# Kernel optimization log

Measured on AMD Instinct MI355X. Metric: run time of the kernel, lower is better.

The kernel has to match this reference:

```python
import jax, jax.numpy as jnp
import numpy as np

K = 1.0        # Lorentz manifold curvature parameter
EPS = 1e-7     # arccosh argument clamp (geoopt float32 eps)


def projx(x):
    # Project onto the hyperboloid: x0 = sqrt(K + ||x_1:||^2)
    rest = x[..., 1:]
    x0 = jnp.sqrt(K + jnp.sum(rest * rest, axis=-1, keepdims=True))
    return jnp.concatenate([x0, rest], axis=-1)


def setup_inputs() -> dict:
    key = jax.random.key(0)
    k1, k2 = jax.random.split(key)
    B, C, D = 16384, 2048, 512
    x = jax.random.normal(k1, (B, D), dtype=jnp.float32)
    # ManifoldParameter: random_normal with std = 1/sqrt(n_dim)
    points = jax.random.normal(k2, (C, D), dtype=jnp.float32) * (1.0 / np.sqrt(D))
    return {"x": x, "points": points}


def reference(x, points):
    xp = projx(x)        # (B, D) on hyperboloid
    pp = projx(points)   # (C, D) on hyperboloid
    # Minkowski inner <x,p>_L = -x0*p0 + sum_{i>0} x_i p_i = x.p - 2*x0*p0
    # Computed as a GEMM plus a rank-1 correction (avoids (B,C,D) intermediate).
    inner = xp @ pp.T - 2.0 * jnp.outer(xp[:, 0], pp[:, 0])  # (B, C)
    d = jnp.sqrt(K) * jnp.arccosh(jnp.maximum(-inner / K, 1.0 + EPS))
    return -d  # (B, C) negative Riemannian distances (class logits)
```

## Files before the change

### kernel.cpp

```cpp
#include <hip/hip_runtime.h>
#include <hip/hip_bf16.h>
#include <stdint.h>

#define B_ROWS 16384
#define C_ROWS 2048
#define D_FULL 512
#define KP     512

#define BM 128
#define BN 128
#define BK 64

typedef __attribute__((ext_vector_type(8))) short bf16x8;
typedef __attribute__((ext_vector_type(4))) float f32x4;

typedef __attribute__((address_space(1))) void glb_void;
typedef __attribute__((address_space(3))) void lds_void;

__device__ __forceinline__ void gld16(const void* g, void* l) {
    __builtin_amdgcn_global_load_lds((glb_void*)(uintptr_t)g,
                                     (lds_void*)(uintptr_t)l, 16, 0, 0);
}

__global__ __launch_bounds__(256) void prep_kernel(
    const float* __restrict__ x, const float* __restrict__ pts,
    unsigned short* __restrict__ Abf, unsigned short* __restrict__ Bbf,
    float* __restrict__ xn, float* __restrict__ pn)
{
    int row = blockIdx.x;
    const float* src;
    unsigned short* dst;
    float* nrm;
    if (row < B_ROWS) {
        src = x + (size_t)row * D_FULL;
        dst = Abf + (size_t)row * KP;
        nrm = xn + row;
    } else {
        int r = row - B_ROWS;
        src = pts + (size_t)r * D_FULL;
        dst = Bbf + (size_t)r * KP;
        nrm = pn + r;
    }
    int t = threadIdx.x;
    float v0 = src[2 * t + 1];
    float v1 = (t < 255) ? src[2 * t + 2] : 0.0f;
    __hip_bfloat16 b0 = __float2bfloat16(v0);
    __hip_bfloat16 b1 = __float2bfloat16(v1);
    union { unsigned short u[2]; unsigned int w; } pack;
    pack.u[0] = *(unsigned short*)&b0;
    pack.u[1] = *(unsigned short*)&b1;
    *(unsigned int*)&dst[2 * t] = pack.w;
    float ss = v0 * v0 + v1 * v1;
    #pragma unroll
    for (int off = 32; off > 0; off >>= 1) ss += __shfl_down(ss, off);
    __shared__ float red[4];
    if ((t & 63) == 0) red[t >> 6] = ss;
    __syncthreads();
    if (t == 0) nrm[0] = sqrtf(1.0f + red[0] + red[1] + red[2] + red[3]);
}

__global__ __launch_bounds__(256, 2) void gemm_kernel(
    const unsigned short* __restrict__ A,
    const unsigned short* __restrict__ Bm,
    const float* __restrict__ xn, const float* __restrict__ pn,
    float* __restrict__ out)
{
    __shared__ unsigned short As[2][BM * BK];
    __shared__ unsigned short Bs[2][BN * BK];

    const int tid  = threadIdx.x;
    const int wave = tid >> 6;
    const int lane = tid & 63;
    const int wm   = wave >> 1;
    const int wn   = wave & 1;
    const int lrow = lane & 15;
    const int quad = lane >> 4;

    const int bm0 = blockIdx.x * BM;
    const int bn0 = blockIdx.y * BN;

    const int srow = wave * 32 + (lane >> 3);
    const int scol = (((lane & 7) ^ ((lane >> 3) & 7)) << 3);

    const unsigned short* gA = A  + (size_t)(bm0 + srow) * KP + scol;
    const unsigned short* gB = Bm + (size_t)(bn0 + srow) * KP + scol;

    f32x4 acc[4][4] = {};

    #pragma unroll
    for (int i = 0; i < 4; ++i) {
        gld16(gA + (size_t)(i * 8) * KP, &As[0][(wave * 32 + i * 8) * BK]);
        gld16(gB + (size_t)(i * 8) * KP, &Bs[0][(wave * 32 + i * 8) * BK]);
    }

    #pragma unroll 2
    for (int it = 0; it < KP / BK; ++it) {
        const int buf = it & 1;
        __syncthreads();
        if (it + 1 < KP / BK) {
            const int k1 = (it + 1) * BK;
            #pragma unroll
            for (int i = 0; i < 4; ++i) {
                gld16(gA + (size_t)(i * 8) * KP + k1, &As[buf ^ 1][(wave * 32 + i * 8) * BK]);
                gld16(gB + (size_t)(i * 8) * KP + k1, &Bs[buf ^ 1][(wave * 32 + i * 8) * BK]);
            }
        }
        #pragma unroll
        for (int kk = 0; kk < BK; kk += 32) {
            const int ch0 = kk >> 3;
            bf16x8 af[4], bfr[4];
            #pragma unroll
            for (int mi = 0; mi < 4; ++mi) {
                int r = wm * 64 + mi * 16 + lrow;
                af[mi] = *(const bf16x8*)&As[buf][r * BK + (((ch0 + quad) ^ (lrow & 7)) << 3)];
            }
            #pragma unroll
            for (int ni = 0; ni < 4; ++ni) {
                int r = wn * 64 + ni * 16 + lrow;
                bfr[ni] = *(const bf16x8*)&Bs[buf][r * BK + (((ch0 + quad) ^ (lrow & 7)) << 3)];
            }
            #pragma unroll
            for (int mi = 0; mi < 4; ++mi)
                #pragma unroll
                for (int ni = 0; ni < 4; ++ni)
                    acc[mi][ni] = __builtin_amdgcn_mfma_f32_16x16x32_bf16(
                        af[mi], bfr[ni], acc[mi][ni], 0, 0, 0);
        }
    }

    float pv[4];
    #pragma unroll
    for (int ni = 0; ni < 4; ++ni)
        pv[ni] = pn[bn0 + wn * 64 + ni * 16 + lrow];

    #pragma unroll
    for (int mi = 0; mi < 4; ++mi) {
        #pragma unroll
        for (int r = 0; r < 4; ++r) {
            int row = bm0 + wm * 64 + mi * 16 + quad * 4 + r;
            float xv = xn[row];
            size_t base = (size_t)row * C_ROWS + bn0 + wn * 64 + lrow;
            #pragma unroll
            for (int ni = 0; ni < 4; ++ni) {
                float z = fmaf(xv, pv[ni], -acc[mi][ni][r]);
                z = fmaxf(z, 1.0f + 1e-7f);
                out[base + ni * 16] = -__logf(z + __fsqrt_rn(z * z - 1.0f));
            }
        }
    }
}

extern "C" void kernel_launch(void* const* d_in, const int* in_sizes, int n_in,
                              void* d_out, int out_size, void* d_ws, size_t ws_size,
                              hipStream_t stream) {
    const float* x   = (const float*)d_in[0];
    const float* pts = (const float*)d_in[1];
    float* out = (float*)d_out;

    char* ws = (char*)d_ws;
    unsigned short* Abf = (unsigned short*)ws;
    unsigned short* Bbf = (unsigned short*)(ws + (size_t)B_ROWS * KP * 2);
    float* xn = (float*)(ws + (size_t)(B_ROWS + C_ROWS) * KP * 2);
    float* pn = (float*)((char*)xn + (size_t)B_ROWS * 4);
    (void)in_sizes; (void)n_in; (void)out_size; (void)ws_size;

    prep_kernel<<<B_ROWS + C_ROWS, 256, 0, stream>>>(x, pts, Abf, Bbf, xn, pn);

    dim3 grid(B_ROWS / BM, C_ROWS / BN);
    gemm_kernel<<<grid, 256, 0, stream>>>(Abf, Bbf, xn, pn, out);
}
```

Measured before the change: 192.1 us.

## Use 256x256 tiles with 4-stage LDS pipeline and vectorized prep

Raises the GEMM block tile to 256x256 with 8 waves. A 4-stage global-to-LDS ring at BK=32 replaces the double buffer, with explicit vmcnt waits, barriers, sched barriers and setprio around the MFMA bursts, and the A/B prefetches are split across the two compute halves. The aim is more reuse per loaded byte and better overlap of loads with MFMA work. The prep kernel now handles one row per wave with float4 loads and 16-byte bf16 stores, dropping the block-level shared reduction. In exchange, LDS use grows to 128KB per block, which likely limits occupancy to one block per CU, and the hand-tuned wait counts are fragile.

```diff
diff --git a/kernel.cpp b/kernel.cpp
--- a/kernel.cpp
+++ b/kernel.cpp
@@ -7,9 +7,9 @@
 #define D_FULL 512
 #define KP     512
 
-#define BM 128
-#define BN 128
-#define BK 64
+#define BM 256
+#define BN 256
+#define BK 32
 
 typedef __attribute__((ext_vector_type(8))) short bf16x8;
 typedef __attribute__((ext_vector_type(4))) float f32x4;
@@ -21,13 +21,23 @@
     __builtin_amdgcn_global_load_lds((glb_void*)(uintptr_t)g,
                                      (lds_void*)(uintptr_t)l, 16, 0, 0);
 }
+
+#define WAITV8 asm volatile("s_waitcnt vmcnt(8)" ::: "memory")
+#define WAITV4 asm volatile("s_waitcnt vmcnt(4)" ::: "memory")
+#define WAITV0 asm volatile("s_waitcnt vmcnt(0)" ::: "memory")
+#define WAITL  asm volatile("s_waitcnt lgkmcnt(0)" ::: "memory")
+#define SBAR   __builtin_amdgcn_s_barrier()
+#define SCHEDB __builtin_amdgcn_sched_barrier(0)
 
 __global__ __launch_bounds__(256) void prep_kernel(
     const float* __restrict__ x, const float* __restrict__ pts,
     unsigned short* __restrict__ Abf, unsigned short* __restrict__ Bbf,
     float* __restrict__ xn, float* __restrict__ pn)
 {
-    int row = blockIdx.x;
+    const int wave = threadIdx.x >> 6;
+    const int l    = threadIdx.x & 63;
+    const int row  = blockIdx.x * 4 + wave;
+
     const float* src;
     unsigned short* dst;
     float* nrm;
@@ -36,96 +46,128 @@
         dst = Abf + (size_t)row * KP;
         nrm = xn + row;
     } else {
-        int r = row - B_ROWS;
+        const int r = row - B_ROWS;
         src = pts + (size_t)r * D_FULL;
         dst = Bbf + (size_t)r * KP;
         nrm = pn + r;
     }
-    int t = threadIdx.x;
-    float v0 = src[2 * t + 1];
-    float v1 = (t < 255) ? src[2 * t + 2] : 0.0f;
-    __hip_bfloat16 b0 = __float2bfloat16(v0);
-    __hip_bfloat16 b1 = __float2bfloat16(v1);
-    union { unsigned short u[2]; unsigned int w; } pack;
-    pack.u[0] = *(unsigned short*)&b0;
-    pack.u[1] = *(unsigned short*)&b1;
-    *(unsigned int*)&dst[2 * t] = pack.w;
-    float ss = v0 * v0 + v1 * v1;
+
+    const float4 a = *(const float4*)&src[8 * l];
+    const float4 b = *(const float4*)&src[8 * l + 4];
+    float nx = __shfl_down(a.x, 1);
+    if (l == 63) nx = 0.0f;
+
+    float v[8] = {a.y, a.z, a.w, b.x, b.y, b.z, b.w, nx};
+    float ss = 0.0f;
+    union { unsigned short us[8]; uint4 q; } pk;
+    #pragma unroll
+    for (int j = 0; j < 8; ++j) {
+        ss += v[j] * v[j];
+        __hip_bfloat16 h = __float2bfloat16(v[j]);
+        pk.us[j] = *(unsigned short*)&h;
+    }
+    *(uint4*)&dst[8 * l] = pk.q;
+
     #pragma unroll
     for (int off = 32; off > 0; off >>= 1) ss += __shfl_down(ss, off);
-    __shared__ float red[4];
-    if ((t & 63) == 0) red[t >> 6] = ss;
-    __syncthreads();
-    if (t == 0) nrm[0] = sqrtf(1.0f + red[0] + red[1] + red[2] + red[3]);
-}
-
-__global__ __launch_bounds__(256, 2) void gemm_kernel(
+    if (l == 0) nrm[0] = sqrtf(1.0f + ss);
+}
+
+__global__ __launch_bounds__(512, 2) void gemm_kernel(
     const unsigned short* __restrict__ A,
     const unsigned short* __restrict__ Bm,
     const float* __restrict__ xn, const float* __restrict__ pn,
     float* __restrict__ out)
 {
-    __shared__ unsigned short As[2][BM * BK];
-    __shared__ unsigned short Bs[2][BN * BK];
+    __shared__ unsigned short As[4][8192];
+    __shared__ unsigned short Bs[4][8192];
 
     const int tid  = threadIdx.x;
     const int wave = tid >> 6;
     const int lane = tid & 63;
-    const int wm   = wave >> 1;
-    const int wn   = wave & 1;
+    const int wm   = wave >> 2;
+    const int wn   = wave & 3;
     const int lrow = lane & 15;
     const int quad = lane >> 4;
 
     const int bm0 = blockIdx.x * BM;
     const int bn0 = blockIdx.y * BN;
 
-    const int srow = wave * 32 + (lane >> 3);
-    const int scol = (((lane & 7) ^ ((lane >> 3) & 7)) << 3);
-
-    const unsigned short* gA = A  + (size_t)(bm0 + srow) * KP + scol;
-    const unsigned short* gB = Bm + (size_t)(bn0 + srow) * KP + scol;
-
-    f32x4 acc[4][4] = {};
-
-    #pragma unroll
-    for (int i = 0; i < 4; ++i) {
-        gld16(gA + (size_t)(i * 8) * KP, &As[0][(wave * 32 + i * 8) * BK]);
-        gld16(gB + (size_t)(i * 8) * KP, &Bs[0][(wave * 32 + i * 8) * BK]);
-    }
-
-    #pragma unroll 2
-    for (int it = 0; it < KP / BK; ++it) {
-        const int buf = it & 1;
-        __syncthreads();
-        if (it + 1 < KP / BK) {
-            const int k1 = (it + 1) * BK;
+    const int P  = tid >> 3;
+    const int u  = tid & 7;
+    const int v  = u ^ (P & 7);
+    const int sc = (v >> 1) << 3;
+    const int rb = 2 * P + (v & 1);
+
+    const unsigned short* gA0 = A  + (size_t)(bm0 + rb) * KP + sc;
+    const unsigned short* gA1 = gA0 + (size_t)128 * KP;
+    const unsigned short* gB0 = Bm + (size_t)(bn0 + rb) * KP + sc;
+    const unsigned short* gB1 = gB0 + (size_t)128 * KP;
+
+    #pragma unroll
+    for (int t = 0; t < 3; ++t) {
+        gld16(gA0 + t * BK, &As[t][wave * 512]);
+        gld16(gA1 + t * BK, &As[t][4096 + wave * 512]);
+        gld16(gB0 + t * BK, &Bs[t][wave * 512]);
+        gld16(gB1 + t * BK, &Bs[t][4096 + wave * 512]);
+    }
+
+    const int ccs  = (((quad << 1) | (lrow & 1)) ^ (lrow >> 1)) << 3;
+    const int aoff = (wm * 64 + (lrow >> 1)) * 64 + ccs;
+    const int boff = (wn * 32 + (lrow >> 1)) * 64 + ccs;
+
+    f32x4 acc[8][4] = {};
+
+    #pragma unroll
+    for (int t = 0; t < KP / BK; ++t) {
+        const int s  = t & 3;
+        const int ps = (t + 3) & 3;
+
+        if (t <= 13)      WAITV8;
+        else if (t == 14) WAITV4;
+        else              WAITV0;
+        SBAR; SCHEDB;
+
+        bf16x8 af[4], bfr[4];
+        #pragma unroll
+        for (int mi = 0; mi < 4; ++mi)
+            af[mi] = *(const bf16x8*)&As[s][aoff + mi * 512];
+        #pragma unroll
+        for (int ni = 0; ni < 4; ++ni)
+            bfr[ni] = *(const bf16x8*)&Bs[s][boff + ni * 512];
+        if (t + 3 < KP / BK) {
+            gld16(gA0 + (t + 3) * BK, &As[ps][wave * 512]);
+            gld16(gA1 + (t + 3) * BK, &As[ps][4096 + wave * 512]);
+        }
+        SBAR;
+        WAITL; SCHEDB;
+        __builtin_amdgcn_s_setprio(1);
+        #pragma unroll
+        for (int mi = 0; mi < 4; ++mi)
             #pragma unroll
-            for (int i = 0; i < 4; ++i) {
-                gld16(gA + (size_t)(i * 8) * KP + k1, &As[buf ^ 1][(wave * 32 + i * 8) * BK]);
-                gld16(gB + (size_t)(i * 8) * KP + k1, &Bs[buf ^ 1][(wave * 32 + i * 8) * BK]);
-            }
+            for (int ni = 0; ni < 4; ++ni)
+                acc[mi][ni] = __builtin_amdgcn_mfma_f32_16x16x32_bf16(
+                    af[mi], bfr[ni], acc[mi][ni], 0, 0, 0);
+        __builtin_amdgcn_s_setprio(0);
+        SBAR;
+
+        #pragma unroll
+        for (int mi = 0; mi < 4; ++mi)
+            af[mi] = *(const bf16x8*)&As[s][aoff + (mi + 4) * 512];
+        if (t + 3 < KP / BK) {
+            gld16(gB0 + (t + 3) * BK, &Bs[ps][wave * 512]);
+            gld16(gB1 + (t + 3) * BK, &Bs[ps][4096 + wave * 512]);
         }
-        #pragma unroll
-        for (int kk = 0; kk < BK; kk += 32) {
-            const int ch0 = kk >> 3;
-            bf16x8 af[4], bfr[4];
+        SBAR;
+        WAITL; SCHEDB;
+        __builtin_amdgcn_s_setprio(1);
+        #pragma unroll
+        for (int mi = 0; mi < 4; ++mi)
             #pragma unroll
-            for (int mi = 0; mi < 4; ++mi) {
-                int r = wm * 64 + mi * 16 + lrow;
-                af[mi] = *(const bf16x8*)&As[buf][r * BK + (((ch0 + quad) ^ (lrow & 7)) << 3)];
-            }
-            #pragma unroll
-            for (int ni = 0; ni < 4; ++ni) {
-                int r = wn * 64 + ni * 16 + lrow;
-                bfr[ni] = *(const bf16x8*)&Bs[buf][r * BK + (((ch0 + quad) ^ (lrow & 7)) << 3)];
-            }
-            #pragma unroll
-            for (int mi = 0; mi < 4; ++mi)
-                #pragma unroll
-                for (int ni = 0; ni < 4; ++ni)
-                    acc[mi][ni] = __builtin_amdgcn_mfma_f32_16x16x32_bf16(
-                        af[mi], bfr[ni], acc[mi][ni], 0, 0, 0);
-        }
+            for (int ni = 0; ni < 4; ++ni)
+                acc[mi + 4][ni] = __builtin_amdgcn_mfma_f32_16x16x32_bf16(
+                    af[mi], bfr[ni], acc[mi + 4][ni], 0, 0, 0);
+        __builtin_amdgcn_s_setprio(0);
     }
 
     float pv[4];
@@ -134,12 +176,12 @@
         pv[ni] = pn[bn0 + wn * 64 + ni * 16 + lrow];
 
     #pragma unroll
-    for (int mi = 0; mi < 4; ++mi) {
+    for (int mi = 0; mi < 8; ++mi) {
         #pragma unroll
         for (int r = 0; r < 4; ++r) {
-            int row = bm0 + wm * 64 + mi * 16 + quad * 4 + r;
-            float xv = xn[row];
-            size_t base = (size_t)row * C_ROWS + bn0 + wn * 64 + lrow;
+            const int row = bm0 + wm * 128 + mi * 16 + quad * 4 + r;
+            const float xv = xn[row];
+            const size_t base = (size_t)row * C_ROWS + bn0 + wn * 64 + lrow;
             #pragma unroll
             for (int ni = 0; ni < 4; ++ni) {
                 float z = fmaf(xv, pv[ni], -acc[mi][ni][r]);
@@ -164,8 +206,8 @@
     float* pn = (float*)((char*)xn + (size_t)B_ROWS * 4);
     (void)in_sizes; (void)n_in; (void)out_size; (void)ws_size;
 
-    prep_kernel<<<B_ROWS + C_ROWS, 256, 0, stream>>>(x, pts, Abf, Bbf, xn, pn);
+    prep_kernel<<<(B_ROWS + C_ROWS) / 4, 256, 0, stream>>>(x, pts, Abf, Bbf, xn, pn);
 
     dim3 grid(B_ROWS / BM, C_ROWS / BN);
-    gemm_kernel<<<grid, 256, 0, stream>>>(Abf, Bbf, xn, pn, out);
-}
+    gemm_kernel<<<grid, 512, 0, stream>>>(Abf, Bbf, xn, pn, out);
+}
```

Result: slower. 196.1 us (+2.1%).
